# Kernel tuning notes

Hardware: AMD Instinct MI355X
Metric: run time of the kernel (lower is better)

Reference implementation:

```python
import jax, jax.numpy as jnp
import numpy as np

B, S, D, H, HD = 4, 1024, 512, 8, 64  # batch, seq_len, hidden_dim, n_heads, head_dim
N_DIL = min(5, H)


def _head_masks(seq_len: int, n_heads: int) -> jnp.ndarray:
    """Log-sparse banded+dilated masks, shape [n_heads, S, S] (bool)."""
    i = jnp.arange(seq_len)
    diff = jnp.abs(i[:, None] - i[None, :])  # [S, S]
    masks = jnp.stack([
        (diff <= 2 ** h) | (diff % (2 ** (h + 1)) == 0)
        for h in range(N_DIL)
    ])  # [N_DIL, S, S]
    idx = [min(h, N_DIL - 1) for h in range(n_heads)]
    return masks[jnp.asarray(idx)]  # [H, S, S]


def setup_inputs() -> dict:
    key = jax.random.key(0)
    ks = jax.random.split(key, 9)
    sc = 0.02
    return {
        "x": jax.random.normal(ks[0], (B, S, D), jnp.float32),
        "Wq": jax.random.normal(ks[1], (H, D, HD), jnp.float32) * sc,
        "bq": jax.random.normal(ks[2], (H, HD), jnp.float32) * sc,
        "Wk": jax.random.normal(ks[3], (H, D, HD), jnp.float32) * sc,
        "bk": jax.random.normal(ks[4], (H, HD), jnp.float32) * sc,
        "Wv": jax.random.normal(ks[5], (H, D, HD), jnp.float32) * sc,
        "bv": jax.random.normal(ks[6], (H, HD), jnp.float32) * sc,
        "Wo": jax.random.normal(ks[7], (D, D), jnp.float32) * sc,
        "bo": jax.random.normal(ks[8], (D,), jnp.float32) * sc,
    }


def reference(x, Wq, bq, Wk, bk, Wv, bv, Wo, bo):
    b, s, d = x.shape
    h, _, hd = Wq.shape
    # Per-head projections (batched over heads).
    q = jnp.einsum("bsd,hde->bhse", x, Wq) + bq[None, :, None, :]
    k = jnp.einsum("bsd,hde->bhse", x, Wk) + bk[None, :, None, :]
    v = jnp.einsum("bsd,hde->bhse", x, Wv) + bv[None, :, None, :]
    scores = jnp.einsum("bhse,bhte->bhst", q, k) / (hd ** 0.5)
    mask = _head_masks(s, h)  # [H, S, S] bool; diagonal always allowed
    scores = jnp.where(mask[None], scores, -jnp.inf)
    probs = jax.nn.softmax(scores, axis=-1)  # dropout is identity in eval
    out = jnp.einsum("bhst,bhte->bhse", probs, v)
    concat = out.transpose(0, 2, 1, 3).reshape(b, s, d)  # heads concatenated
    return concat @ Wo + bo
```

## Files before the change

kernel.cpp:

```cpp
#include <hip/hip_runtime.h>

typedef unsigned short u16;
typedef unsigned int u32;
typedef __attribute__((ext_vector_type(8))) __bf16 bf16x8;
typedef __attribute__((ext_vector_type(4))) float f32x4;
typedef __attribute__((ext_vector_type(16))) float f32x16;
typedef __attribute__((ext_vector_type(4))) u32 u32x4;

#if __has_builtin(__builtin_amdgcn_exp2f)
#define EXP2F(x) __builtin_amdgcn_exp2f(x)
#else
#define EXP2F(x) exp2f(x)
#endif

#define SC_Q 0.18033688011112042f

static __device__ __forceinline__ u16 f2bf(float f) {
  unsigned u = __builtin_bit_cast(unsigned, f);
  u += 0x7fffu + ((u >> 16) & 1u);
  return (u16)(u >> 16);
}
static __device__ __forceinline__ float bf2f(u16 v) {
  return __builtin_bit_cast(float, (u32)v << 16);
}

static __device__ __forceinline__ f32x4 mfma16(bf16x8 a, bf16x8 b, f32x4 c) {
  return __builtin_amdgcn_mfma_f32_16x16x32_bf16(a, b, c, 0, 0, 0);
}
static __device__ __forceinline__ f32x16 mfma32(bf16x8 a, bf16x8 b, f32x16 c) {
  return __builtin_amdgcn_mfma_f32_32x32x16_bf16(a, b, c, 0, 0, 0);
}

static __device__ __forceinline__ u32 cvtpk(float lo, float hi_) {
  u32 r;
  asm("v_cvt_pk_bf16_f32 %0, %1, %2" : "=v"(r) : "v"(lo), "v"(hi_));
  return r;
}

static __device__ __forceinline__ void barrier_raw() {
  asm volatile("" ::: "memory");
  __builtin_amdgcn_s_barrier();
  asm volatile("" ::: "memory");
}

static __device__ __forceinline__ void gload_lds16(const u16* g, u16* l) {
  __builtin_amdgcn_global_load_lds((const __attribute__((address_space(1))) u32*)g,
                                   (__attribute__((address_space(3))) u32*)l, 16, 0, 0);
}

__global__ void pack_w_kernel(const float* __restrict__ Wq, const float* __restrict__ Wk,
                              const float* __restrict__ Wv, const float* __restrict__ Wo,
                              const float* __restrict__ bq, const float* __restrict__ bk,
                              const float* __restrict__ bv, u16* __restrict__ BTqkv,
                              u16* __restrict__ BTo, float* __restrict__ bqkv) {
  int idx = blockIdx.x * 256 + threadIdx.x;
  if (idx < 1536 * 512) {
    int n = idx >> 9, d = idx & 511;
    int t = n >> 9, rem = n & 511;
    int h = rem >> 6, e = rem & 63;
    const float* W = (t == 0) ? Wq : ((t == 1) ? Wk : Wv);
    float sc = (t == 0) ? SC_Q : 1.0f;
    BTqkv[idx] = f2bf(W[((size_t)h * 512 + d) * 64 + e] * sc);
  } else if (idx < 1536 * 512 + 512 * 512) {
    int j = idx - 1536 * 512;
    int n = j >> 9, d = j & 511;
    BTo[j] = f2bf(Wo[(size_t)d * 512 + n]);
  } else if (idx < 1536 * 512 + 512 * 512 + 1536) {
    int j = idx - (1536 * 512 + 512 * 512);
    int t = j >> 9, rem = j & 511;
    float v = (t == 0 ? bq : (t == 1 ? bk : bv))[rem];
    bqkv[j] = v * (t == 0 ? SC_Q : 1.0f);
  }
}

__global__ __launch_bounds__(256) void gemm_qkv_kernel(const float* __restrict__ X,
                                                       const u16* __restrict__ BT,
                                                       const float* __restrict__ bias,
                                                       u16* __restrict__ QK,
                                                       u16* __restrict__ Vt) {
  __shared__ __align__(16) u16 Al[2][128 * 64];
  __shared__ __align__(16) u16 Bl[2][64 * 64];
  const int K = 512;
  const int tid = threadIdx.x;
  const int w = tid >> 6, lane = tid & 63, g = lane >> 4, i = lane & 15;
  const int m0 = blockIdx.y * 128, n0 = blockIdx.x * 64;
  const int wr = (w >> 1) * 64, wc = (w & 1) * 32;

  f32x4 acc[4][2];
#pragma unroll
  for (int a = 0; a < 4; ++a)
#pragma unroll
    for (int b = 0; b < 2; ++b) acc[a][b] = f32x4{0.f, 0.f, 0.f, 0.f};

  const float* xg[4];
#pragma unroll
  for (int it = 0; it < 4; ++it) {
    const int slot = it * 256 + tid;
    xg[it] = X + (size_t)(m0 + (slot >> 3)) * K + (slot & 7) * 8;
  }
  const u16* bgp[2];
#pragma unroll
  for (int it = 0; it < 2; ++it) {
    const int slot = it * 256 + tid;
    bgp[it] = BT + (size_t)(n0 + (slot >> 3)) * K + (slot & 7) * 8;
  }

  float4 a0[4], a1[4];
#pragma unroll
  for (int it = 0; it < 4; ++it) {
    a0[it] = *reinterpret_cast<const float4*>(xg[it]);
    a1[it] = *reinterpret_cast<const float4*>(xg[it] + 4);
  }
#pragma unroll
  for (int it = 0; it < 2; ++it) gload_lds16(bgp[it], &Bl[0][(it * 256 + tid) * 8]);
  asm volatile("s_waitcnt vmcnt(2)" ::: "memory");
#pragma unroll
  for (int it = 0; it < 4; ++it) {
    u32x4 pk = {cvtpk(a0[it].x, a0[it].y), cvtpk(a0[it].z, a0[it].w),
                cvtpk(a1[it].x, a1[it].y), cvtpk(a1[it].z, a1[it].w)};
    *reinterpret_cast<u32x4*>(&Al[0][(it * 256 + tid) * 8]) = pk;
  }
  asm volatile("s_waitcnt lgkmcnt(0)" ::: "memory");

  int cur = 0;
  for (int t = 0; t < 8; ++t) {
    const int k0 = t * 64;
    if (t < 7) {
#pragma unroll
      for (int it = 0; it < 4; ++it) {
        a0[it] = *reinterpret_cast<const float4*>(xg[it] + k0 + 64);
        a1[it] = *reinterpret_cast<const float4*>(xg[it] + k0 + 68);
      }
#pragma unroll
      for (int it = 0; it < 2; ++it)
        gload_lds16(bgp[it] + k0 + 64, &Bl[cur ^ 1][(it * 256 + tid) * 8]);
      asm volatile("s_waitcnt vmcnt(10)" ::: "memory");
    } else {
      asm volatile("s_waitcnt vmcnt(0)" ::: "memory");
    }
    barrier_raw();
#pragma unroll
    for (int ks = 0; ks < 2; ++ks) {
      bf16x8 af[4], bf[2];
#pragma unroll
      for (int mf = 0; mf < 4; ++mf)
        af[mf] = *reinterpret_cast<const bf16x8*>(
            &Al[cur][(wr + mf * 16 + i) * 64 + ks * 32 + 8 * g]);
#pragma unroll
      for (int nf = 0; nf < 2; ++nf)
        bf[nf] = *reinterpret_cast<const bf16x8*>(
            &Bl[cur][(wc + nf * 16 + i) * 64 + ks * 32 + 8 * g]);
#pragma unroll
      for (int mf = 0; mf < 4; ++mf)
#pragma unroll
        for (int nf = 0; nf < 2; ++nf) acc[mf][nf] = mfma16(af[mf], bf[nf], acc[mf][nf]);
    }
    if (t < 7) {
      asm volatile("s_waitcnt vmcnt(2)" ::: "memory");
#pragma unroll
      for (int it = 0; it < 4; ++it) {
        u32x4 pk = {cvtpk(a0[it].x, a0[it].y), cvtpk(a0[it].z, a0[it].w),
                    cvtpk(a1[it].x, a1[it].y), cvtpk(a1[it].z, a1[it].w)};
        *reinterpret_cast<u32x4*>(&Al[cur ^ 1][(it * 256 + tid) * 8]) = pk;
      }
      asm volatile("s_waitcnt lgkmcnt(0)" ::: "memory");
    }
    barrier_raw();
    cur ^= 1;
  }

  if (n0 < 1024) {
#pragma unroll
    for (int nf = 0; nf < 2; ++nf) {
      const int col = n0 + wc + nf * 16 + i;
      const float bb = bias[col];
#pragma unroll
      for (int mf = 0; mf < 4; ++mf) {
#pragma unroll
        for (int r = 0; r < 4; ++r) {
          const int row = m0 + wr + mf * 16 + 4 * g + r;
          QK[(size_t)row * 1024 + col] = f2bf(acc[mf][nf][r] + bb);
        }
      }
    }
  } else {
    const int b = m0 >> 10;
    const int s0b = (m0 & 1023) + wr;
#pragma unroll
    for (int nf = 0; nf < 2; ++nf) {
      const int col = n0 + wc + nf * 16 + i;
      const float bb = bias[col];
      const int vcol = col - 1024;
#pragma unroll
      for (int mf = 0; mf < 4; ++mf) {
        u16 pk[4];
#pragma unroll
        for (int r = 0; r < 4; ++r) pk[r] = f2bf(acc[mf][nf][r] + bb);
        const int ss = s0b + mf * 16 + 4 * g;
        *reinterpret_cast<uint2*>(&Vt[(size_t)(b * 512 + vcol) * 1024 + ss]) =
            *reinterpret_cast<const uint2*>(pk);
      }
    }
  }
}

__global__ __launch_bounds__(256) void gemm_out_kernel(const u16* __restrict__ A,
                                                       const u16* __restrict__ BT,
                                                       const float* __restrict__ bias,
                                                       float* __restrict__ Cf) {
  __shared__ __align__(16) u16 Al[2][64 * 64];
  __shared__ __align__(16) u16 Bl[2][64 * 64];
  const int K = 512;
  const int tid = threadIdx.x;
  const int w = tid >> 6, lane = tid & 63, g = lane >> 4, i = lane & 15;
  const int m0 = blockIdx.y * 64, n0 = blockIdx.x * 64;
  const int wr = (w >> 1) * 32, wc = (w & 1) * 32;

  f32x4 acc[2][2];
#pragma unroll
  for (int a = 0; a < 2; ++a)
#pragma unroll
    for (int b = 0; b < 2; ++b) acc[a][b] = f32x4{0.f, 0.f, 0.f, 0.f};

  const u16* agp[2];
  const u16* bgp[2];
#pragma unroll
  for (int it = 0; it < 2; ++it) {
    const int slot = it * 256 + tid;
    agp[it] = A + (size_t)(m0 + (slot >> 3)) * K + (slot & 7) * 8;
    bgp[it] = BT + (size_t)(n0 + (slot >> 3)) * K + (slot & 7) * 8;
  }

#define OSTAGE(bi, k0)                                              \
  do {                                                              \
    _Pragma("unroll") for (int it = 0; it < 2; ++it) {              \
      gload_lds16(agp[it] + (k0), &Al[bi][(it * 256 + tid) * 8]);   \
      gload_lds16(bgp[it] + (k0), &Bl[bi][(it * 256 + tid) * 8]);   \
    }                                                               \
  } while (0)

  OSTAGE(0, 0);
  int cur = 0;
  for (int t = 0; t < 8; ++t) {
    if (t < 7) {
      OSTAGE(cur ^ 1, t * 64 + 64);
      asm volatile("s_waitcnt vmcnt(4)" ::: "memory");
    } else {
      asm volatile("s_waitcnt vmcnt(0)" ::: "memory");
    }
    barrier_raw();
#pragma unroll
    for (int ks = 0; ks < 2; ++ks) {
      bf16x8 af[2], bf[2];
#pragma unroll
      for (int mf = 0; mf < 2; ++mf)
        af[mf] = *reinterpret_cast<const bf16x8*>(
            &Al[cur][(wr + mf * 16 + i) * 64 + ks * 32 + 8 * g]);
#pragma unroll
      for (int nf = 0; nf < 2; ++nf)
        bf[nf] = *reinterpret_cast<const bf16x8*>(
            &Bl[cur][(wc + nf * 16 + i) * 64 + ks * 32 + 8 * g]);
#pragma unroll
      for (int mf = 0; mf < 2; ++mf)
#pragma unroll
        for (int nf = 0; nf < 2; ++nf) acc[mf][nf] = mfma16(af[mf], bf[nf], acc[mf][nf]);
    }
    barrier_raw();
    cur ^= 1;
  }
#undef OSTAGE

#pragma unroll
  for (int nf = 0; nf < 2; ++nf) {
    const int col = n0 + wc + nf * 16 + i;
    const float bb = bias[col];
#pragma unroll
    for (int mf = 0; mf < 2; ++mf) {
#pragma unroll
      for (int r = 0; r < 4; ++r) {
        const int row = m0 + wr + mf * 16 + 4 * g + r;
        Cf[(size_t)row * 512 + col] = acc[mf][nf][r] + bb;
      }
    }
  }
}

__global__ __launch_bounds__(256) void attn3_kernel(const u16* __restrict__ QK,
                                                    const u16* __restrict__ Vt,
                                                    u16* __restrict__ Opart16,
                                                    float* __restrict__ mlpart) {
  __shared__ __align__(16) u16 Kl[2][4096];
  __shared__ __align__(16) u16 Vl[2][4096];

  const int tid = threadIdx.x;
  const int w = tid >> 6, lane = tid & 63;
  const int col = lane & 31, hi = lane >> 5;
  const int h = blockIdx.x;
  const int zz = blockIdx.z;
  const int b = zz >> 2, s = zz & 3;
  const int bh = b * 8 + h;
  const int q0w = blockIdx.y * 128 + w * 32;
  const int kvlo = s * 256;
  const int hm = (h < 4) ? h : 4;
  const int band = 1 << hm;
  const int modm = (2 << hm) - 1;
  const int qrow = q0w + col;

  bf16x8 qf[4];
  const size_t qoff = (size_t)(b * 1024 + qrow) * 1024 + h * 64 + 8 * hi;
#pragma unroll
  for (int et = 0; et < 4; ++et)
    qf[et] = *reinterpret_cast<const bf16x8*>(QK + qoff + 16 * et);

  float bias[16];
#pragma unroll
  for (int r = 0; r < 16; ++r) {
    int c = (r & 3) + 8 * (r >> 2) + 4 * hi;
    bias[r] = (((qrow - c) & modm) == 0) ? 0.f : -1e30f;
  }

  f32x16 accO0 = {}, accO1 = {};
  float m_run = -1e30f, l_run = 0.f;

  const int slot0 = tid, slot1 = tid + 256;
  const int kj0 = slot0 >> 3, keb0 = (slot0 & 7) ^ (kj0 & 7);
  const int kj1 = slot1 >> 3, keb1 = (slot1 & 7) ^ (kj1 & 7);
  const u16* kg0 = QK + (size_t)(b * 1024 + kj0) * 1024 + 512 + h * 64 + keb0 * 8;
  const u16* kg1 = QK + (size_t)(b * 1024 + kj1) * 1024 + 512 + h * 64 + keb1 * 8;
  const u16* vg0 = Vt + (size_t)(bh * 64 + kj0) * 1024 + keb0 * 8;
  const u16* vg1 = Vt + (size_t)(bh * 64 + kj1) * 1024 + keb1 * 8;

#define STAGE(bi, kv0)                                                  \
  do {                                                                  \
    gload_lds16(kg0 + (size_t)(kv0) * 1024, &Kl[bi][slot0 * 8]);        \
    gload_lds16(kg1 + (size_t)(kv0) * 1024, &Kl[bi][slot1 * 8]);        \
    gload_lds16(vg0 + (kv0), &Vl[bi][slot0 * 8]);                       \
    gload_lds16(vg1 + (kv0), &Vl[bi][slot1 * 8]);                       \
  } while (0)

  STAGE(0, kvlo);
  int buf = 0;

  for (int t = 0; t < 4; ++t) {
    const int kv0 = kvlo + t * 64;
    if (t < 3) {
      STAGE(buf ^ 1, kv0 + 64);
      asm volatile("s_waitcnt vmcnt(4)" ::: "memory");
    } else {
      asm volatile("s_waitcnt vmcnt(0)" ::: "memory");
    }
    barrier_raw();

    const u16* Kb = Kl[buf];
    const u16* Vb = Vl[buf];

    f32x16 s0 = {}, s1 = {};
    __builtin_amdgcn_s_setprio(1);
#pragma unroll
    for (int et = 0; et < 4; ++et) {
      const int sw = ((2 * et + hi) ^ (col & 7)) << 3;
      bf16x8 kf0 = *reinterpret_cast<const bf16x8*>(&Kb[col * 64 + sw]);
      bf16x8 kf1 = *reinterpret_cast<const bf16x8*>(&Kb[(col + 32) * 64 + sw]);
      s0 = mfma32(kf0, qf[et], s0);
      s1 = mfma32(kf1, qf[et], s1);
    }
    __builtin_amdgcn_s_setprio(0);

    float p[32];
    const int dq = qrow - kv0;
    const bool near = (q0w <= kv0 + 63 + band) && (kv0 <= q0w + 31 + band);
    if (near) {
#pragma unroll
      for (int r = 0; r < 16; ++r) {
        const int c = (r & 3) + 8 * (r >> 2) + 4 * hi;
        int d0 = dq - c, d1 = d0 - 32;
        d0 = d0 < 0 ? -d0 : d0;
        d1 = d1 < 0 ? -d1 : d1;
        p[r] = (d0 <= band) ? s0[r] : s0[r] + bias[r];
        p[r + 16] = (d1 <= band) ? s1[r] : s1[r] + bias[r];
      }
    } else {
#pragma unroll
      for (int r = 0; r < 16; ++r) {
        p[r] = s0[r] + bias[r];
        p[r + 16] = s1[r] + bias[r];
      }
    }

    float tr[16];
#pragma unroll
    for (int j = 0; j < 16; ++j) tr[j] = fmaxf(p[j], p[j + 16]);
#pragma unroll
    for (int st = 8; st >= 1; st >>= 1)
#pragma unroll
      for (int j = 0; j < st; ++j) tr[j] = fmaxf(tr[j], tr[j + st]);
    float mu = fmaxf(tr[0], __shfl_xor(tr[0], 32));

    if (__any(mu > m_run + 8.f)) {
      float mn = fmaxf(m_run, mu);
      float corr = EXP2F(m_run - mn);
      m_run = mn;
      l_run *= corr;
#pragma unroll
      for (int j = 0; j < 16; ++j) {
        accO0[j] *= corr;
        accO1[j] *= corr;
      }
    }

#pragma unroll
    for (int j = 0; j < 32; ++j) p[j] = EXP2F(p[j] - m_run);
    float ts[16];
#pragma unroll
    for (int j = 0; j < 16; ++j) ts[j] = p[j] + p[j + 16];
#pragma unroll
    for (int st = 8; st >= 1; st >>= 1)
#pragma unroll
      for (int j = 0; j < st; ++j) ts[j] += ts[j + st];
    l_run += ts[0] + __shfl_xor(ts[0], 32);

#pragma unroll
    for (int kt = 0; kt < 4; ++kt) {
      const float* pp = (kt < 2) ? p : p + 16;
      const int R = (kt & 1) * 8;
      u32 A0 = cvtpk(pp[R + 0], pp[R + 1]);
      u32 A1 = cvtpk(pp[R + 2], pp[R + 3]);
      u32 B0 = cvtpk(pp[R + 4], pp[R + 5]);
      u32 B1 = cvtpk(pp[R + 6], pp[R + 7]);
      u32 xA0 = __shfl_xor(A0, 32), xA1 = __shfl_xor(A1, 32);
      u32 xB0 = __shfl_xor(B0, 32), xB1 = __shfl_xor(B1, 32);
      u32 w0 = hi ? xB0 : A0;
      u32 w1 = hi ? xB1 : A1;
      u32 w2 = hi ? B0 : xA0;
      u32 w3 = hi ? B1 : xA1;
      u32x4 pu = {w0, w1, w2, w3};
      bf16x8 paf = __builtin_bit_cast(bf16x8, pu);
      const int jb = 2 * kt + hi;
      __builtin_amdgcn_s_setprio(1);
      {
        const int erow = col;
        bf16x8 vf = *reinterpret_cast<const bf16x8*>(&Vb[erow * 64 + ((jb ^ (erow & 7)) << 3)]);
        accO0 = mfma32(paf, vf, accO0);
      }
      {
        const int erow = 32 + col;
        bf16x8 vf = *reinterpret_cast<const bf16x8*>(&Vb[erow * 64 + ((jb ^ (erow & 7)) << 3)]);
        accO1 = mfma32(paf, vf, accO1);
      }
      __builtin_amdgcn_s_setprio(0);
    }

    barrier_raw();
    buf ^= 1;
  }
#undef STAGE

  const size_t obase = (size_t)(s * 32 + bh) * 1024 + q0w;
  if (lane < 32) {
    float2 ml2 = {m_run, l_run};
    *reinterpret_cast<float2*>(&mlpart[(obase + col) * 2]) = ml2;
  }
#pragma unroll
  for (int r = 0; r < 16; ++r) {
    const int c = (r & 3) + 8 * (r >> 2) + 4 * hi;
    u16* orow = Opart16 + (obase + c) * 64;
    orow[col] = f2bf(accO0[r]);
    orow[32 + col] = f2bf(accO1[r]);
  }
}

__global__ __launch_bounds__(256) void attn_combine_kernel(const u16* __restrict__ Opart16,
                                                           const float* __restrict__ mlpart,
                                                           u16* __restrict__ Cc) {
  const int gid = blockIdx.x * 256 + threadIdx.x;
  const int rg = gid >> 4;
  const int e0 = (gid & 15) * 4;
  float m[4], l[4];
#pragma unroll
  for (int s2 = 0; s2 < 4; ++s2) {
    float2 ml2 = *reinterpret_cast<const float2*>(&mlpart[((size_t)s2 * 32768 + rg) * 2]);
    m[s2] = ml2.x;
    l[s2] = ml2.y;
  }
  const float M = fmaxf(fmaxf(m[0], m[1]), fmaxf(m[2], m[3]));
  float L = 0.f, wsc[4];
#pragma unroll
  for (int s2 = 0; s2 < 4; ++s2) {
    wsc[s2] = EXP2F(m[s2] - M);
    L += l[s2] * wsc[s2];
  }
  float o0 = 0.f, o1 = 0.f, o2 = 0.f, o3 = 0.f;
#pragma unroll
  for (int s2 = 0; s2 < 4; ++s2) {
    uint2 raw =
        *reinterpret_cast<const uint2*>(&Opart16[((size_t)s2 * 32768 + rg) * 64 + e0]);
    o0 += bf2f((u16)(raw.x & 0xffff)) * wsc[s2];
    o1 += bf2f((u16)(raw.x >> 16)) * wsc[s2];
    o2 += bf2f((u16)(raw.y & 0xffff)) * wsc[s2];
    o3 += bf2f((u16)(raw.y >> 16)) * wsc[s2];
  }
  const float inv = 1.0f / L;
  const int bh = rg >> 10, qr = rg & 1023;
  u16 ob[4] = {f2bf(o0 * inv), f2bf(o1 * inv), f2bf(o2 * inv), f2bf(o3 * inv)};
  *reinterpret_cast<uint2*>(&Cc[(size_t)((bh >> 3) * 1024 + qr) * 512 + (bh & 7) * 64 + e0]) =
      *reinterpret_cast<const uint2*>(ob);
}

extern "C" void kernel_launch(void* const* d_in, const int* in_sizes, int n_in,
                              void* d_out, int out_size, void* d_ws, size_t ws_size,
                              hipStream_t stream) {
  const float* x = (const float*)d_in[0];
  const float* Wq = (const float*)d_in[1];
  const float* bq = (const float*)d_in[2];
  const float* Wk = (const float*)d_in[3];
  const float* bk = (const float*)d_in[4];
  const float* Wv = (const float*)d_in[5];
  const float* bv = (const float*)d_in[6];
  const float* Wo = (const float*)d_in[7];
  const float* bo = (const float*)d_in[8];
  float* out = (float*)d_out;

  char* ws = (char*)d_ws;
  u16* BTqkv = (u16*)(ws + (4u << 20));
  u16* BTo = (u16*)(ws + (6u << 20));
  float* bqkv = (float*)(ws + (7u << 20));
  u16* QK = (u16*)(ws + (8u << 20));
  u16* Cc = (u16*)(ws + (17u << 20));
  u16* Vt = (u16*)(ws + (21u << 20));
  u16* Opart16 = (u16*)(ws + (32u << 20));
  float* mlpart = (float*)(ws + (64u << 20));

  const int NW = 1536 * 512 + 512 * 512 + 1536;
  pack_w_kernel<<<(NW + 255) / 256, 256, 0, stream>>>(Wq, Wk, Wv, Wo, bq, bk, bv, BTqkv,
                                                      BTo, bqkv);

  gemm_qkv_kernel<<<dim3(24, 32), 256, 0, stream>>>(x, BTqkv, bqkv, QK, Vt);

  attn3_kernel<<<dim3(8, 8, 16), 256, 0, stream>>>(QK, Vt, Opart16, mlpart);
  attn_combine_kernel<<<2048, 256, 0, stream>>>(Opart16, mlpart, Cc);

  gemm_out_kernel<<<dim3(8, 64), 256, 0, stream>>>(Cc, BTo, bo, out);
}
```

Baseline: 68.58 us.

## Split sparse heads into dilated and band kernels using permuted V layout

For heads 4-7, where the dilation stride is 32, the work moves out of the generic attention kernel into two specialised kernels. One handles the dilated pattern by gathering the same-residue keys, using a new residue-permuted copy of V written by the QKV GEMM. The other handles the local band within a 64-key window. The combine kernel then merges only two partials for these heads instead of four. This is meant to cut the wasted masked work of the original kernel, at the cost of extra scattered writes of V, two extra launches, and tricky partial indexing.

```diff
diff --git a/kernel.cpp b/kernel.cpp
--- a/kernel.cpp
+++ b/kernel.cpp
@@ -77,7 +77,8 @@
                                                        const u16* __restrict__ BT,
                                                        const float* __restrict__ bias,
                                                        u16* __restrict__ QK,
-                                                       u16* __restrict__ Vt) {
+                                                       u16* __restrict__ Vtl,
+                                                       u16* __restrict__ Vtp) {
   __shared__ __align__(16) u16 Al[2][128 * 64];
   __shared__ __align__(16) u16 Bl[2][64 * 64];
   const int K = 512;
@@ -191,14 +192,24 @@
       const int col = n0 + wc + nf * 16 + i;
       const float bb = bias[col];
       const int vcol = col - 1024;
+      const int hh = vcol >> 6;
+      const int hmm = (hh < 4) ? hh : 4;
+      const int Mlog = hmm + 1;
+      const int NcH = 1024 >> Mlog;
+      const size_t rowb = (size_t)(b * 512 + vcol) * 1024;
 #pragma unroll
       for (int mf = 0; mf < 4; ++mf) {
         u16 pk[4];
 #pragma unroll
         for (int r = 0; r < 4; ++r) pk[r] = f2bf(acc[mf][nf][r] + bb);
         const int ss = s0b + mf * 16 + 4 * g;
-        *reinterpret_cast<uint2*>(&Vt[(size_t)(b * 512 + vcol) * 1024 + ss]) =
-            *reinterpret_cast<const uint2*>(pk);
+        *reinterpret_cast<uint2*>(&Vtl[rowb + ss]) = *reinterpret_cast<const uint2*>(pk);
+#pragma unroll
+        for (int r = 0; r < 4; ++r) {
+          const int seq = ss + r;
+          const int pidx = (seq & ((1 << Mlog) - 1)) * NcH + (seq >> Mlog);
+          Vtp[rowb + pidx] = pk[r];
+        }
       }
     }
   }
@@ -330,7 +341,7 @@
   const u16* vg0 = Vt + (size_t)(bh * 64 + kj0) * 1024 + keb0 * 8;
   const u16* vg1 = Vt + (size_t)(bh * 64 + kj1) * 1024 + keb1 * 8;
 
-#define STAGE(bi, kv0)                                                  \
+#define STAGE3(bi, kv0)                                                 \
   do {                                                                  \
     gload_lds16(kg0 + (size_t)(kv0) * 1024, &Kl[bi][slot0 * 8]);        \
     gload_lds16(kg1 + (size_t)(kv0) * 1024, &Kl[bi][slot1 * 8]);        \
@@ -338,13 +349,13 @@
     gload_lds16(vg1 + (kv0), &Vl[bi][slot1 * 8]);                       \
   } while (0)
 
-  STAGE(0, kvlo);
+  STAGE3(0, kvlo);
   int buf = 0;
 
   for (int t = 0; t < 4; ++t) {
     const int kv0 = kvlo + t * 64;
     if (t < 3) {
-      STAGE(buf ^ 1, kv0 + 64);
+      STAGE3(buf ^ 1, kv0 + 64);
       asm volatile("s_waitcnt vmcnt(4)" ::: "memory");
     } else {
       asm volatile("s_waitcnt vmcnt(0)" ::: "memory");
@@ -453,7 +464,7 @@
     barrier_raw();
     buf ^= 1;
   }
-#undef STAGE
+#undef STAGE3
 
   const size_t obase = (size_t)(s * 32 + bh) * 1024 + q0w;
   if (lane < 32) {
@@ -464,6 +475,219 @@
   for (int r = 0; r < 16; ++r) {
     const int c = (r & 3) + 8 * (r >> 2) + 4 * hi;
     u16* orow = Opart16 + (obase + c) * 64;
+    orow[col] = f2bf(accO0[r]);
+    orow[32 + col] = f2bf(accO1[r]);
+  }
+}
+
+#define SOFTMAX_PV(p, Vb, VS, toff, NKT)                                              \
+  do {                                                                                \
+    float tr[16];                                                                     \
+    _Pragma("unroll") for (int j = 0; j < 16; ++j) tr[j] = fmaxf(p[j], p[j + 16]);    \
+    _Pragma("unroll") for (int st = 8; st >= 1; st >>= 1)                             \
+        _Pragma("unroll") for (int j = 0; j < st; ++j) tr[j] = fmaxf(tr[j], tr[j + st]); \
+    float mu = fmaxf(tr[0], __shfl_xor(tr[0], 32));                                   \
+    if (__any(mu > m_run + 8.f)) {                                                    \
+      float mn = fmaxf(m_run, mu);                                                    \
+      float corr = EXP2F(m_run - mn);                                                 \
+      m_run = mn;                                                                     \
+      l_run *= corr;                                                                  \
+      _Pragma("unroll") for (int j = 0; j < 16; ++j) {                                \
+        accO0[j] *= corr;                                                             \
+        accO1[j] *= corr;                                                             \
+      }                                                                               \
+    }                                                                                 \
+    _Pragma("unroll") for (int j = 0; j < 32; ++j) p[j] = EXP2F(p[j] - m_run);        \
+    float ts[16];                                                                     \
+    _Pragma("unroll") for (int j = 0; j < 16; ++j) ts[j] = p[j] + p[j + 16];          \
+    _Pragma("unroll") for (int st = 8; st >= 1; st >>= 1)                             \
+        _Pragma("unroll") for (int j = 0; j < st; ++j) ts[j] += ts[j + st];           \
+    l_run += ts[0] + __shfl_xor(ts[0], 32);                                           \
+    _Pragma("unroll") for (int kt = 0; kt < (NKT); ++kt) {                            \
+      const float* pp = (kt < 2) ? p : p + 16;                                        \
+      const int R = (kt & 1) * 8;                                                     \
+      u32 A0 = cvtpk(pp[R + 0], pp[R + 1]);                                           \
+      u32 A1 = cvtpk(pp[R + 2], pp[R + 3]);                                           \
+      u32 B0 = cvtpk(pp[R + 4], pp[R + 5]);                                           \
+      u32 B1 = cvtpk(pp[R + 6], pp[R + 7]);                                           \
+      u32 xA0 = __shfl_xor(A0, 32), xA1 = __shfl_xor(A1, 32);                         \
+      u32 xB0 = __shfl_xor(B0, 32), xB1 = __shfl_xor(B1, 32);                         \
+      u32 w0 = hi ? xB0 : A0;                                                         \
+      u32 w1 = hi ? xB1 : A1;                                                         \
+      u32 w2 = hi ? B0 : xA0;                                                         \
+      u32 w3 = hi ? B1 : xA1;                                                         \
+      u32x4 pu = {w0, w1, w2, w3};                                                    \
+      bf16x8 paf = __builtin_bit_cast(bf16x8, pu);                                    \
+      const int jb = 2 * kt + hi;                                                     \
+      {                                                                               \
+        const int erow = col;                                                         \
+        bf16x8 vf = *reinterpret_cast<const bf16x8*>(&Vb[erow * (VS) + (toff) + (jb << 3)]); \
+        accO0 = mfma32(paf, vf, accO0);                                               \
+      }                                                                               \
+      {                                                                               \
+        const int erow = 32 + col;                                                    \
+        bf16x8 vf = *reinterpret_cast<const bf16x8*>(&Vb[erow * (VS) + (toff) + (jb << 3)]); \
+        accO1 = mfma32(paf, vf, accO1);                                               \
+      }                                                                               \
+    }                                                                                 \
+  } while (0)
+
+__global__ __launch_bounds__(256) void attnD_kernel(const u16* __restrict__ QK,
+                                                    const u16* __restrict__ Vtp,
+                                                    u16* __restrict__ Opart16,
+                                                    float* __restrict__ mlpart) {
+  __shared__ __align__(16) u16 Kl[4][32 * 72];
+  __shared__ __align__(16) u16 Vl[4][64 * 40];
+
+  const int tid = threadIdx.x;
+  const int w = tid >> 6, lane = tid & 63;
+  const int col = lane & 31, hi = lane >> 5;
+  const int h = 4 + blockIdx.x;
+  const int qblk = blockIdx.y, b = blockIdx.z;
+  const int M = 32;
+  const int cls = qblk * 4 + w;
+  const int bh = b * 8 + h;
+
+  for (int sl = lane; sl < 256; sl += 64) {
+    const int kj = sl >> 3, eb = sl & 7;
+    const int physk = cls + kj * M;
+    bf16x8 kreg = *reinterpret_cast<const bf16x8*>(
+        QK + (size_t)(b * 1024 + physk) * 1024 + 512 + h * 64 + eb * 8);
+    *reinterpret_cast<bf16x8*>(&Kl[w][kj * 72 + eb * 8]) = kreg;
+  }
+  for (int sl = lane; sl < 256; sl += 64) {
+    const int e = sl >> 2, tb = sl & 3;
+    bf16x8 vreg = *reinterpret_cast<const bf16x8*>(
+        Vtp + (size_t)(b * 512 + h * 64 + e) * 1024 + cls * 32 + tb * 8);
+    *reinterpret_cast<bf16x8*>(&Vl[w][e * 40 + tb * 8]) = vreg;
+  }
+
+  const int physq = cls + col * M;
+  bf16x8 qf[4];
+  const size_t qoff = (size_t)(b * 1024 + physq) * 1024 + h * 64 + 8 * hi;
+#pragma unroll
+  for (int et = 0; et < 4; ++et)
+    qf[et] = *reinterpret_cast<const bf16x8*>(QK + qoff + 16 * et);
+
+  f32x16 accO0 = {}, accO1 = {};
+  float m_run = -1e30f, l_run = 0.f;
+
+  __syncthreads();
+
+  f32x16 s0 = {};
+  __builtin_amdgcn_s_setprio(1);
+#pragma unroll
+  for (int et = 0; et < 4; ++et) {
+    const int sw8 = (2 * et + hi) * 8;
+    bf16x8 kf0 = *reinterpret_cast<const bf16x8*>(&Kl[w][col * 72 + sw8]);
+    s0 = mfma32(kf0, qf[et], s0);
+  }
+  __builtin_amdgcn_s_setprio(0);
+
+  float p[32];
+#pragma unroll
+  for (int r = 0; r < 16; ++r) {
+    p[r] = s0[r];
+    p[r + 16] = -1e30f;
+  }
+  const u16* Vb = &Vl[w][0];
+  SOFTMAX_PV(p, Vb, 40, 0, 2);
+
+  const size_t pb = (size_t)(1 * 32 + bh) * 1024;
+  if (lane < 32) {
+    float2 ml2 = {m_run, l_run};
+    *reinterpret_cast<float2*>(&mlpart[(pb + physq) * 2]) = ml2;
+  }
+#pragma unroll
+  for (int r = 0; r < 16; ++r) {
+    const int cf = (r & 3) + 8 * (r >> 2) + 4 * hi;
+    const int physr = cls + cf * M;
+    u16* orow = Opart16 + (pb + physr) * 64;
+    orow[col] = f2bf(accO0[r]);
+    orow[32 + col] = f2bf(accO1[r]);
+  }
+}
+
+__global__ __launch_bounds__(256) void attnB_kernel(const u16* __restrict__ QK,
+                                                    const u16* __restrict__ Vtl,
+                                                    u16* __restrict__ Opart16,
+                                                    float* __restrict__ mlpart) {
+  __shared__ __align__(16) u16 Kl[4][64 * 72];
+  __shared__ __align__(16) u16 Vl[4][64 * 72];
+
+  const int tid = threadIdx.x;
+  const int w = tid >> 6, lane = tid & 63;
+  const int col = lane & 31, hi = lane >> 5;
+  const int h = 4 + blockIdx.x;
+  const int qt = blockIdx.y, b = blockIdx.z;
+  const int bh = b * 8 + h;
+  const int band = 16;
+  const int q0w = qt * 128 + w * 32;
+  const int qrow = q0w + col;
+  int kw = q0w - 16;
+  kw = kw < 0 ? 0 : (kw > 960 ? 960 : kw);
+
+  for (int sl = tid; sl < 2048; sl += 256) {
+    const int wv = sl >> 9, s9 = sl & 511;
+    int kwv = qt * 128 + wv * 32 - 16;
+    kwv = kwv < 0 ? 0 : (kwv > 960 ? 960 : kwv);
+    const int kj = s9 >> 3, eb = s9 & 7;
+    bf16x8 kreg = *reinterpret_cast<const bf16x8*>(
+        QK + (size_t)(b * 1024 + kwv + kj) * 1024 + 512 + h * 64 + eb * 8);
+    *reinterpret_cast<bf16x8*>(&Kl[wv][kj * 72 + eb * 8]) = kreg;
+    bf16x8 vreg = *reinterpret_cast<const bf16x8*>(
+        Vtl + (size_t)(b * 512 + h * 64 + kj) * 1024 + kwv + eb * 8);
+    *reinterpret_cast<bf16x8*>(&Vl[wv][kj * 72 + eb * 8]) = vreg;
+  }
+
+  bf16x8 qf[4];
+  const size_t qoff = (size_t)(b * 1024 + qrow) * 1024 + h * 64 + 8 * hi;
+#pragma unroll
+  for (int et = 0; et < 4; ++et)
+    qf[et] = *reinterpret_cast<const bf16x8*>(QK + qoff + 16 * et);
+
+  f32x16 accO0 = {}, accO1 = {};
+  float m_run = -1e30f, l_run = 0.f;
+
+  __syncthreads();
+
+  const u16* Kb = &Kl[w][0];
+  const u16* Vb = &Vl[w][0];
+
+  f32x16 s0 = {}, s1 = {};
+  __builtin_amdgcn_s_setprio(1);
+#pragma unroll
+  for (int et = 0; et < 4; ++et) {
+    const int sw8 = (2 * et + hi) * 8;
+    bf16x8 kf0 = *reinterpret_cast<const bf16x8*>(&Kb[col * 72 + sw8]);
+    bf16x8 kf1 = *reinterpret_cast<const bf16x8*>(&Kb[(col + 32) * 72 + sw8]);
+    s0 = mfma32(kf0, qf[et], s0);
+    s1 = mfma32(kf1, qf[et], s1);
+  }
+  __builtin_amdgcn_s_setprio(0);
+
+  float p[32];
+  const int dq = qrow - kw;
+#pragma unroll
+  for (int r = 0; r < 16; ++r) {
+    const int cf = (r & 3) + 8 * (r >> 2) + 4 * hi;
+    const int d0 = dq - cf, d1 = d0 - 32;
+    const int a0 = d0 < 0 ? -d0 : d0;
+    const int a1 = d1 < 0 ? -d1 : d1;
+    p[r] = (a0 >= 1 && a0 <= band) ? s0[r] : -1e30f;
+    p[r + 16] = (a1 >= 1 && a1 <= band) ? s1[r] : -1e30f;
+  }
+  SOFTMAX_PV(p, Vb, 72, 0, 4);
+
+  const size_t pb = (size_t)bh * 1024;
+  if (lane < 32) {
+    float2 ml2 = {m_run, l_run};
+    *reinterpret_cast<float2*>(&mlpart[(pb + qrow) * 2]) = ml2;
+  }
+#pragma unroll
+  for (int r = 0; r < 16; ++r) {
+    const int cf = (r & 3) + 8 * (r >> 2) + 4 * hi;
+    u16* orow = Opart16 + (pb + q0w + cf) * 64;
     orow[col] = f2bf(accO0[r]);
     orow[32 + col] = f2bf(accO1[r]);
   }
@@ -475,32 +699,31 @@
   const int gid = blockIdx.x * 256 + threadIdx.x;
   const int rg = gid >> 4;
   const int e0 = (gid & 15) * 4;
+  const int bh = rg >> 10, qr = rg & 1023;
+  const int h = bh & 7;
+  const int np = (h < 4) ? 4 : 2;
+
   float m[4], l[4];
-#pragma unroll
-  for (int s2 = 0; s2 < 4; ++s2) {
+  for (int s2 = 0; s2 < np; ++s2) {
     float2 ml2 = *reinterpret_cast<const float2*>(&mlpart[((size_t)s2 * 32768 + rg) * 2]);
     m[s2] = ml2.x;
     l[s2] = ml2.y;
   }
-  const float M = fmaxf(fmaxf(m[0], m[1]), fmaxf(m[2], m[3]));
-  float L = 0.f, wsc[4];
-#pragma unroll
-  for (int s2 = 0; s2 < 4; ++s2) {
-    wsc[s2] = EXP2F(m[s2] - M);
-    L += l[s2] * wsc[s2];
-  }
+  float M = m[0];
+  for (int s2 = 1; s2 < np; ++s2) M = fmaxf(M, m[s2]);
+  float L = 0.f;
   float o0 = 0.f, o1 = 0.f, o2 = 0.f, o3 = 0.f;
-#pragma unroll
-  for (int s2 = 0; s2 < 4; ++s2) {
+  for (int s2 = 0; s2 < np; ++s2) {
+    const float wsc = EXP2F(m[s2] - M);
+    L += l[s2] * wsc;
     uint2 raw =
         *reinterpret_cast<const uint2*>(&Opart16[((size_t)s2 * 32768 + rg) * 64 + e0]);
-    o0 += bf2f((u16)(raw.x & 0xffff)) * wsc[s2];
-    o1 += bf2f((u16)(raw.x >> 16)) * wsc[s2];
-    o2 += bf2f((u16)(raw.y & 0xffff)) * wsc[s2];
-    o3 += bf2f((u16)(raw.y >> 16)) * wsc[s2];
+    o0 += bf2f((u16)(raw.x & 0xffff)) * wsc;
+    o1 += bf2f((u16)(raw.x >> 16)) * wsc;
+    o2 += bf2f((u16)(raw.y & 0xffff)) * wsc;
+    o3 += bf2f((u16)(raw.y >> 16)) * wsc;
   }
   const float inv = 1.0f / L;
-  const int bh = rg >> 10, qr = rg & 1023;
   u16 ob[4] = {f2bf(o0 * inv), f2bf(o1 * inv), f2bf(o2 * inv), f2bf(o3 * inv)};
   *reinterpret_cast<uint2*>(&Cc[(size_t)((bh >> 3) * 1024 + qr) * 512 + (bh & 7) * 64 + e0]) =
       *reinterpret_cast<const uint2*>(ob);
@@ -526,17 +749,20 @@
   float* bqkv = (float*)(ws + (7u << 20));
   u16* QK = (u16*)(ws + (8u << 20));
   u16* Cc = (u16*)(ws + (17u << 20));
-  u16* Vt = (u16*)(ws + (21u << 20));
+  u16* Vtl = (u16*)(ws + (21u << 20));
+  u16* Vtp = (u16*)(ws + (25u << 20));
   u16* Opart16 = (u16*)(ws + (32u << 20));
-  float* mlpart = (float*)(ws + (64u << 20));
+  float* mlpart = (float*)(ws + (56u << 20));
 
   const int NW = 1536 * 512 + 512 * 512 + 1536;
   pack_w_kernel<<<(NW + 255) / 256, 256, 0, stream>>>(Wq, Wk, Wv, Wo, bq, bk, bv, BTqkv,
                                                       BTo, bqkv);
 
-  gemm_qkv_kernel<<<dim3(24, 32), 256, 0, stream>>>(x, BTqkv, bqkv, QK, Vt);
-
-  attn3_kernel<<<dim3(8, 8, 16), 256, 0, stream>>>(QK, Vt, Opart16, mlpart);
+  gemm_qkv_kernel<<<dim3(24, 32), 256, 0, stream>>>(x, BTqkv, bqkv, QK, Vtl, Vtp);
+
+  attn3_kernel<<<dim3(4, 8, 16), 256, 0, stream>>>(QK, Vtl, Opart16, mlpart);
+  attnD_kernel<<<dim3(4, 8, 4), 256, 0, stream>>>(QK, Vtp, Opart16, mlpart);
+  attnB_kernel<<<dim3(4, 8, 4), 256, 0, stream>>>(QK, Vtl, Opart16, mlpart);
   attn_combine_kernel<<<2048, 256, 0, stream>>>(Opart16, mlpart, Cc);
 
   gemm_out_kernel<<<dim3(8, 64), 256, 0, stream>>>(Cc, BTo, bo, out);
```

New measurement: 78.68 us. 1.15x slower.

## Fuse split-KV combine into output GEMM and halve attention KV splits

Applied to the files above, without the earlier changes.

The attention kernel now splits the KV range into 2 chunks of 512 instead of 4 of 256, which halves the partial outputs and the blocks launched. The separate combine kernel is removed. The output-projection GEMM now loads the two partial O tiles plus their max/sum stats directly, merges them in registers, and writes bf16 A tiles into LDS while the B tiles stream in. This removes one launch and the write and read of the combined Cc buffer, but lowers attention parallelism and adds ALU and global-load work inside the GEMM's main loop.

```diff
diff --git a/kernel.cpp b/kernel.cpp
--- a/kernel.cpp
+++ b/kernel.cpp
@@ -77,7 +77,7 @@
                                                        const u16* __restrict__ BT,
                                                        const float* __restrict__ bias,
                                                        u16* __restrict__ QK,
-                                                       u16* __restrict__ Vt) {
+                                                       u16* __restrict__ Vtl) {
   __shared__ __align__(16) u16 Al[2][128 * 64];
   __shared__ __align__(16) u16 Bl[2][64 * 64];
   const int K = 512;
@@ -191,95 +191,14 @@
       const int col = n0 + wc + nf * 16 + i;
       const float bb = bias[col];
       const int vcol = col - 1024;
+      const size_t rowb = (size_t)(b * 512 + vcol) * 1024;
 #pragma unroll
       for (int mf = 0; mf < 4; ++mf) {
         u16 pk[4];
 #pragma unroll
         for (int r = 0; r < 4; ++r) pk[r] = f2bf(acc[mf][nf][r] + bb);
         const int ss = s0b + mf * 16 + 4 * g;
-        *reinterpret_cast<uint2*>(&Vt[(size_t)(b * 512 + vcol) * 1024 + ss]) =
-            *reinterpret_cast<const uint2*>(pk);
-      }
-    }
-  }
-}
-
-__global__ __launch_bounds__(256) void gemm_out_kernel(const u16* __restrict__ A,
-                                                       const u16* __restrict__ BT,
-                                                       const float* __restrict__ bias,
-                                                       float* __restrict__ Cf) {
-  __shared__ __align__(16) u16 Al[2][64 * 64];
-  __shared__ __align__(16) u16 Bl[2][64 * 64];
-  const int K = 512;
-  const int tid = threadIdx.x;
-  const int w = tid >> 6, lane = tid & 63, g = lane >> 4, i = lane & 15;
-  const int m0 = blockIdx.y * 64, n0 = blockIdx.x * 64;
-  const int wr = (w >> 1) * 32, wc = (w & 1) * 32;
-
-  f32x4 acc[2][2];
-#pragma unroll
-  for (int a = 0; a < 2; ++a)
-#pragma unroll
-    for (int b = 0; b < 2; ++b) acc[a][b] = f32x4{0.f, 0.f, 0.f, 0.f};
-
-  const u16* agp[2];
-  const u16* bgp[2];
-#pragma unroll
-  for (int it = 0; it < 2; ++it) {
-    const int slot = it * 256 + tid;
-    agp[it] = A + (size_t)(m0 + (slot >> 3)) * K + (slot & 7) * 8;
-    bgp[it] = BT + (size_t)(n0 + (slot >> 3)) * K + (slot & 7) * 8;
-  }
-
-#define OSTAGE(bi, k0)                                              \
-  do {                                                              \
-    _Pragma("unroll") for (int it = 0; it < 2; ++it) {              \
-      gload_lds16(agp[it] + (k0), &Al[bi][(it * 256 + tid) * 8]);   \
-      gload_lds16(bgp[it] + (k0), &Bl[bi][(it * 256 + tid) * 8]);   \
-    }                                                               \
-  } while (0)
-
-  OSTAGE(0, 0);
-  int cur = 0;
-  for (int t = 0; t < 8; ++t) {
-    if (t < 7) {
-      OSTAGE(cur ^ 1, t * 64 + 64);
-      asm volatile("s_waitcnt vmcnt(4)" ::: "memory");
-    } else {
-      asm volatile("s_waitcnt vmcnt(0)" ::: "memory");
-    }
-    barrier_raw();
-#pragma unroll
-    for (int ks = 0; ks < 2; ++ks) {
-      bf16x8 af[2], bf[2];
-#pragma unroll
-      for (int mf = 0; mf < 2; ++mf)
-        af[mf] = *reinterpret_cast<const bf16x8*>(
-            &Al[cur][(wr + mf * 16 + i) * 64 + ks * 32 + 8 * g]);
-#pragma unroll
-      for (int nf = 0; nf < 2; ++nf)
-        bf[nf] = *reinterpret_cast<const bf16x8*>(
-            &Bl[cur][(wc + nf * 16 + i) * 64 + ks * 32 + 8 * g]);
-#pragma unroll
-      for (int mf = 0; mf < 2; ++mf)
-#pragma unroll
-        for (int nf = 0; nf < 2; ++nf) acc[mf][nf] = mfma16(af[mf], bf[nf], acc[mf][nf]);
-    }
-    barrier_raw();
-    cur ^= 1;
-  }
-#undef OSTAGE
-
-#pragma unroll
-  for (int nf = 0; nf < 2; ++nf) {
-    const int col = n0 + wc + nf * 16 + i;
-    const float bb = bias[col];
-#pragma unroll
-    for (int mf = 0; mf < 2; ++mf) {
-#pragma unroll
-      for (int r = 0; r < 4; ++r) {
-        const int row = m0 + wr + mf * 16 + 4 * g + r;
-        Cf[(size_t)row * 512 + col] = acc[mf][nf][r] + bb;
+        *reinterpret_cast<uint2*>(&Vtl[rowb + ss]) = *reinterpret_cast<const uint2*>(pk);
       }
     }
   }
@@ -297,10 +216,10 @@
   const int col = lane & 31, hi = lane >> 5;
   const int h = blockIdx.x;
   const int zz = blockIdx.z;
-  const int b = zz >> 2, s = zz & 3;
+  const int b = zz >> 1, s = zz & 1;
   const int bh = b * 8 + h;
   const int q0w = blockIdx.y * 128 + w * 32;
-  const int kvlo = s * 256;
+  const int kvlo = s * 512;
   const int hm = (h < 4) ? h : 4;
   const int band = 1 << hm;
   const int modm = (2 << hm) - 1;
@@ -330,7 +249,7 @@
   const u16* vg0 = Vt + (size_t)(bh * 64 + kj0) * 1024 + keb0 * 8;
   const u16* vg1 = Vt + (size_t)(bh * 64 + kj1) * 1024 + keb1 * 8;
 
-#define STAGE(bi, kv0)                                                  \
+#define STAGE3(bi, kv0)                                                 \
   do {                                                                  \
     gload_lds16(kg0 + (size_t)(kv0) * 1024, &Kl[bi][slot0 * 8]);        \
     gload_lds16(kg1 + (size_t)(kv0) * 1024, &Kl[bi][slot1 * 8]);        \
@@ -338,13 +257,13 @@
     gload_lds16(vg1 + (kv0), &Vl[bi][slot1 * 8]);                       \
   } while (0)
 
-  STAGE(0, kvlo);
+  STAGE3(0, kvlo);
   int buf = 0;
 
-  for (int t = 0; t < 4; ++t) {
+  for (int t = 0; t < 8; ++t) {
     const int kv0 = kvlo + t * 64;
-    if (t < 3) {
-      STAGE(buf ^ 1, kv0 + 64);
+    if (t < 7) {
+      STAGE3(buf ^ 1, kv0 + 64);
       asm volatile("s_waitcnt vmcnt(4)" ::: "memory");
     } else {
       asm volatile("s_waitcnt vmcnt(0)" ::: "memory");
@@ -453,7 +372,7 @@
     barrier_raw();
     buf ^= 1;
   }
-#undef STAGE
+#undef STAGE3
 
   const size_t obase = (size_t)(s * 32 + bh) * 1024 + q0w;
   if (lane < 32) {
@@ -469,41 +388,138 @@
   }
 }
 
-__global__ __launch_bounds__(256) void attn_combine_kernel(const u16* __restrict__ Opart16,
-                                                           const float* __restrict__ mlpart,
-                                                           u16* __restrict__ Cc) {
-  const int gid = blockIdx.x * 256 + threadIdx.x;
-  const int rg = gid >> 4;
-  const int e0 = (gid & 15) * 4;
-  float m[4], l[4];
-#pragma unroll
-  for (int s2 = 0; s2 < 4; ++s2) {
-    float2 ml2 = *reinterpret_cast<const float2*>(&mlpart[((size_t)s2 * 32768 + rg) * 2]);
-    m[s2] = ml2.x;
-    l[s2] = ml2.y;
-  }
-  const float M = fmaxf(fmaxf(m[0], m[1]), fmaxf(m[2], m[3]));
-  float L = 0.f, wsc[4];
-#pragma unroll
-  for (int s2 = 0; s2 < 4; ++s2) {
-    wsc[s2] = EXP2F(m[s2] - M);
-    L += l[s2] * wsc[s2];
-  }
-  float o0 = 0.f, o1 = 0.f, o2 = 0.f, o3 = 0.f;
-#pragma unroll
-  for (int s2 = 0; s2 < 4; ++s2) {
-    uint2 raw =
-        *reinterpret_cast<const uint2*>(&Opart16[((size_t)s2 * 32768 + rg) * 64 + e0]);
-    o0 += bf2f((u16)(raw.x & 0xffff)) * wsc[s2];
-    o1 += bf2f((u16)(raw.x >> 16)) * wsc[s2];
-    o2 += bf2f((u16)(raw.y & 0xffff)) * wsc[s2];
-    o3 += bf2f((u16)(raw.y >> 16)) * wsc[s2];
-  }
-  const float inv = 1.0f / L;
-  const int bh = rg >> 10, qr = rg & 1023;
-  u16 ob[4] = {f2bf(o0 * inv), f2bf(o1 * inv), f2bf(o2 * inv), f2bf(o3 * inv)};
-  *reinterpret_cast<uint2*>(&Cc[(size_t)((bh >> 3) * 1024 + qr) * 512 + (bh & 7) * 64 + e0]) =
-      *reinterpret_cast<const uint2*>(ob);
+__global__ __launch_bounds__(256) void gemm_out_kernel(const u16* __restrict__ Opart16,
+                                                       const float* __restrict__ mlpart,
+                                                       const u16* __restrict__ BT,
+                                                       const float* __restrict__ bias,
+                                                       float* __restrict__ Cf) {
+  __shared__ __align__(16) u16 Al[2][64 * 64];
+  __shared__ __align__(16) u16 Bl[2][64 * 64];
+  const int K = 512;
+  const int tid = threadIdx.x;
+  const int w = tid >> 6, lane = tid & 63, g = lane >> 4, i = lane & 15;
+  const int m0 = blockIdx.y * 64, n0 = blockIdx.x * 64;
+  const int wr = (w >> 1) * 32, wc = (w & 1) * 32;
+
+  f32x4 acc[2][2];
+#pragma unroll
+  for (int a = 0; a < 2; ++a)
+#pragma unroll
+    for (int b = 0; b < 2; ++b) acc[a][b] = f32x4{0.f, 0.f, 0.f, 0.f};
+
+  size_t R0[2];
+  int cb8[2];
+#pragma unroll
+  for (int it = 0; it < 2; ++it) {
+    const int slot = it * 256 + tid;
+    const int r_in = slot >> 3;
+    cb8[it] = (slot & 7) * 8;
+    const int grow = m0 + r_in;
+    const int b2 = grow >> 10, qr = grow & 1023;
+    R0[it] = (size_t)(b2 * 8) * 1024 + qr;
+  }
+  const u16* bgp[2];
+#pragma unroll
+  for (int it = 0; it < 2; ++it) {
+    const int slot = it * 256 + tid;
+    bgp[it] = BT + (size_t)(n0 + (slot >> 3)) * K + (slot & 7) * 8;
+  }
+
+  uint4 aO[2][2];
+  float2 aml[2][2];
+
+#define LOAD_A(t)                                                                     \
+  do {                                                                                \
+    _Pragma("unroll") for (int it = 0; it < 2; ++it) {                                \
+      _Pragma("unroll") for (int s2 = 0; s2 < 2; ++s2) {                              \
+        const size_t rb = R0[it] + (size_t)(s2 * 32 + (t)) * 1024;                    \
+        aO[it][s2] = *reinterpret_cast<const uint4*>(&Opart16[rb * 64 + cb8[it]]);    \
+        aml[it][s2] = *reinterpret_cast<const float2*>(&mlpart[rb * 2]);              \
+      }                                                                               \
+    }                                                                                 \
+  } while (0)
+
+#define COMBINE_WRITE(bi)                                                             \
+  do {                                                                                \
+    _Pragma("unroll") for (int it = 0; it < 2; ++it) {                                \
+      const float mA = aml[it][0].x, lA = aml[it][0].y;                               \
+      const float mB = aml[it][1].x, lB = aml[it][1].y;                               \
+      const float M2 = fmaxf(mA, mB);                                                 \
+      const float wA = EXP2F(mA - M2), wB = EXP2F(mB - M2);                           \
+      const float inv = 1.0f / (lA * wA + lB * wB);                                   \
+      const float sA = wA * inv, sB = wB * inv;                                       \
+      const u32* oa = reinterpret_cast<const u32*>(&aO[it][0]);                       \
+      const u32* ob = reinterpret_cast<const u32*>(&aO[it][1]);                       \
+      float c[8];                                                                     \
+      _Pragma("unroll") for (int q = 0; q < 4; ++q) {                                 \
+        c[2 * q] = bf2f((u16)(oa[q] & 0xffff)) * sA + bf2f((u16)(ob[q] & 0xffff)) * sB; \
+        c[2 * q + 1] = bf2f((u16)(oa[q] >> 16)) * sA + bf2f((u16)(ob[q] >> 16)) * sB; \
+      }                                                                               \
+      u32x4 pk = {cvtpk(c[0], c[1]), cvtpk(c[2], c[3]), cvtpk(c[4], c[5]),            \
+                  cvtpk(c[6], c[7])};                                                 \
+      *reinterpret_cast<u32x4*>(&Al[bi][(it * 256 + tid) * 8]) = pk;                  \
+    }                                                                                 \
+  } while (0)
+
+  LOAD_A(0);
+#pragma unroll
+  for (int it = 0; it < 2; ++it) gload_lds16(bgp[it], &Bl[0][(it * 256 + tid) * 8]);
+  asm volatile("s_waitcnt vmcnt(2)" ::: "memory");
+  COMBINE_WRITE(0);
+  asm volatile("s_waitcnt lgkmcnt(0)" ::: "memory");
+
+  int cur = 0;
+  for (int t = 0; t < 8; ++t) {
+    if (t < 7) {
+      LOAD_A(t + 1);
+#pragma unroll
+      for (int it = 0; it < 2; ++it)
+        gload_lds16(bgp[it] + t * 64 + 64, &Bl[cur ^ 1][(it * 256 + tid) * 8]);
+      asm volatile("s_waitcnt vmcnt(10)" ::: "memory");
+    } else {
+      asm volatile("s_waitcnt vmcnt(0)" ::: "memory");
+    }
+    barrier_raw();
+#pragma unroll
+    for (int ks = 0; ks < 2; ++ks) {
+      bf16x8 af[2], bf[2];
+#pragma unroll
+      for (int mf = 0; mf < 2; ++mf)
+        af[mf] = *reinterpret_cast<const bf16x8*>(
+            &Al[cur][(wr + mf * 16 + i) * 64 + ks * 32 + 8 * g]);
+#pragma unroll
+      for (int nf = 0; nf < 2; ++nf)
+        bf[nf] = *reinterpret_cast<const bf16x8*>(
+            &Bl[cur][(wc + nf * 16 + i) * 64 + ks * 32 + 8 * g]);
+#pragma unroll
+      for (int mf = 0; mf < 2; ++mf)
+#pragma unroll
+        for (int nf = 0; nf < 2; ++nf) acc[mf][nf] = mfma16(af[mf], bf[nf], acc[mf][nf]);
+    }
+    if (t < 7) {
+      asm volatile("s_waitcnt vmcnt(2)" ::: "memory");
+      COMBINE_WRITE(cur ^ 1);
+      asm volatile("s_waitcnt lgkmcnt(0)" ::: "memory");
+    }
+    barrier_raw();
+    cur ^= 1;
+  }
+#undef LOAD_A
+#undef COMBINE_WRITE
+
+#pragma unroll
+  for (int nf = 0; nf < 2; ++nf) {
+    const int col = n0 + wc + nf * 16 + i;
+    const float bb = bias[col];
+#pragma unroll
+    for (int mf = 0; mf < 2; ++mf) {
+#pragma unroll
+      for (int r = 0; r < 4; ++r) {
+        const int row = m0 + wr + mf * 16 + 4 * g + r;
+        Cf[(size_t)row * 512 + col] = acc[mf][nf][r] + bb;
+      }
+    }
+  }
 }
 
 extern "C" void kernel_launch(void* const* d_in, const int* in_sizes, int n_in,
@@ -525,19 +541,17 @@
   u16* BTo = (u16*)(ws + (6u << 20));
   float* bqkv = (float*)(ws + (7u << 20));
   u16* QK = (u16*)(ws + (8u << 20));
-  u16* Cc = (u16*)(ws + (17u << 20));
-  u16* Vt = (u16*)(ws + (21u << 20));
+  u16* Vtl = (u16*)(ws + (21u << 20));
   u16* Opart16 = (u16*)(ws + (32u << 20));
-  float* mlpart = (float*)(ws + (64u << 20));
+  float* mlpart = (float*)(ws + (56u << 20));
 
   const int NW = 1536 * 512 + 512 * 512 + 1536;
   pack_w_kernel<<<(NW + 255) / 256, 256, 0, stream>>>(Wq, Wk, Wv, Wo, bq, bk, bv, BTqkv,
                                                       BTo, bqkv);
 
-  gemm_qkv_kernel<<<dim3(24, 32), 256, 0, stream>>>(x, BTqkv, bqkv, QK, Vt);
-
-  attn3_kernel<<<dim3(8, 8, 16), 256, 0, stream>>>(QK, Vt, Opart16, mlpart);
-  attn_combine_kernel<<<2048, 256, 0, stream>>>(Opart16, mlpart, Cc);
-
-  gemm_out_kernel<<<dim3(8, 64), 256, 0, stream>>>(Cc, BTo, bo, out);
-}
+  gemm_qkv_kernel<<<dim3(24, 32), 256, 0, stream>>>(x, BTqkv, bqkv, QK, Vtl);
+
+  attn3_kernel<<<dim3(8, 8, 8), 256, 0, stream>>>(QK, Vtl, Opart16, mlpart);
+
+  gemm_out_kernel<<<dim3(8, 64), 256, 0, stream>>>(Opart16, mlpart, BTo, bo, out);
+}
```

After: 68.89 us. No clear change (+0.4%).
